# Kernel tuning notes

Measured on AMD Instinct MI355X. Metric: run time of the kernel, lower is better.

Reference implementation:

```python
import jax, jax.numpy as jnp
import numpy as np

B, S, H, NH, L, INTER, WIN = 2, 2048, 512, 8, 4, 2048, 64
HD = H // NH
W1 = WIN // 2          # one-sided window
WB = 2 * W1 + 1        # band width per query
EPS = 1e-12


def layer_norm(x, g, b):
    m = jnp.mean(x, axis=-1, keepdims=True)
    v = jnp.var(x, axis=-1, keepdims=True)
    return (x - m) / jnp.sqrt(v + EPS) * g + b


def setup_inputs() -> dict:
    key = jax.random.key(0)
    ks = jax.random.split(key, 12)
    std = 0.02
    n = lambda k, sh: jax.random.normal(k, sh, jnp.float32) * std
    return {
        "input_embs": jax.random.normal(ks[0], (B, S, H), jnp.float32),
        "attention_mask": jnp.ones((B, S), jnp.float32),
        "pos_emb": n(ks[1], (S, H)),
        "ln_emb_g": jnp.ones((H,), jnp.float32),
        "ln_emb_b": jnp.zeros((H,), jnp.float32),
        "Wq": n(ks[2], (L, H, H)), "bq": jnp.zeros((L, H), jnp.float32),
        "Wk": n(ks[3], (L, H, H)), "bk": jnp.zeros((L, H), jnp.float32),
        "Wv": n(ks[4], (L, H, H)), "bv": jnp.zeros((L, H), jnp.float32),
        "Wo": n(ks[5], (L, H, H)), "bo": jnp.zeros((L, H), jnp.float32),
        "ln1_g": jnp.ones((L, H), jnp.float32), "ln1_b": jnp.zeros((L, H), jnp.float32),
        "Wi": n(ks[6], (L, H, INTER)), "bi": jnp.zeros((L, INTER), jnp.float32),
        "Wo2": n(ks[7], (L, INTER, H)), "bo2": jnp.zeros((L, H), jnp.float32),
        "ln2_g": jnp.ones((L, H), jnp.float32), "ln2_b": jnp.zeros((L, H), jnp.float32),
        "pool_W1": n(ks[8], (H, H)), "pool_b1": jnp.zeros((H,), jnp.float32),
        "pool_W2": n(ks[9], (H, 1)), "pool_b2": jnp.zeros((1,), jnp.float32),
    }


def reference(input_embs, attention_mask, pos_emb, ln_emb_g, ln_emb_b,
              Wq, bq, Wk, bk, Wv, bv, Wo, bo, ln1_g, ln1_b,
              Wi, bi, Wo2, bo2, ln2_g, ln2_b,
              pool_W1, pool_b1, pool_W2, pool_b2):
    # extended additive mask: 0 for attend, -10000 for pad (no global tokens)
    ext = (1.0 - attention_mask) * -10000.0          # [B,S]
    is_masked = ext < 0                              # masked query positions

    # embeddings: input + position, LayerNorm (dropout is identity in eval)
    x = layer_norm(input_embs + pos_emb[None], ln_emb_g, ln_emb_b)

    # sliding-window band indices
    offs = jnp.arange(-W1, W1 + 1)
    idx = jnp.arange(S)[:, None] + offs[None, :]     # [S,WB]
    valid = (idx >= 0) & (idx < S)
    idxc = jnp.clip(idx, 0, S - 1)
    key_bias = ext[:, idxc]                          # [B,S,WB] additive key mask
    scale = 1.0 / jnp.sqrt(jnp.float32(HD))

    def layer(h, p):
        (wq, bq_, wk, bk_, wv, bv_, wo, bo_, g1, b1,
         wi, bi_, wo2, bo2_, g2, b2) = p
        q = (h @ wq + bq_).reshape(B, S, NH, HD) * scale
        k = (h @ wk + bk_).reshape(B, S, NH, HD)
        v = (h @ wv + bv_).reshape(B, S, NH, HD)
        kb = k[:, idxc]                              # [B,S,WB,NH,HD]
        vb = v[:, idxc]
        sc = jnp.einsum('bshd,bswhd->bhsw', q, kb) + key_bias[:, None]
        sc = jnp.where(valid[None, None], sc, -jnp.inf)
        pr = jax.nn.softmax(sc, axis=-1)
        pr = jnp.where(is_masked[:, None, :, None], 0.0, pr)
        ctx = jnp.einsum('bhsw,bswhd->bshd', pr, vb).reshape(B, S, H)
        attn = layer_norm(ctx @ wo + bo_ + h, g1, b1)          # BertSelfOutput
        inter = jax.nn.gelu(attn @ wi + bi_, approximate=False)  # BertIntermediate
        out = layer_norm(inter @ wo2 + bo2_ + attn, g2, b2)      # BertOutput
        return out, None

    params = (Wq, bq, Wk, bk, Wv, bv, Wo, bo, ln1_g, ln1_b,
              Wi, bi, Wo2, bo2, ln2_g, ln2_b)
    x, _ = jax.lax.scan(jax.checkpoint(layer), x, params)

    # AttentionPooling
    e = jnp.tanh(x @ pool_W1 + pool_b1)
    alpha = jnp.exp(e @ pool_W2 + pool_b2) * attention_mask[..., None]  # [B,S,1]
    alpha = alpha / (jnp.sum(alpha, axis=1, keepdims=True) + 1e-8)
    return jnp.einsum('bsh,bs->bh', x, alpha[..., 0])  # [B,H]
```

## Files before the change

### kernel.cpp

```cpp
#include <hip/hip_runtime.h>
#include <hip/hip_bf16.h>
#include <math.h>

#define B_ 2
#define S_ 2048
#define H_ 512
#define NH_ 8
#define HD_ 64
#define L_ 4
#define INTER_ 2048
#define W1_ 32
#define WB_ 65
#define M_ (B_*S_)

typedef __attribute__((ext_vector_type(8))) short short8v;
typedef __attribute__((ext_vector_type(4))) float f32x4;

__device__ __forceinline__ float b2f(ushort u){ return __uint_as_float(((unsigned)u)<<16); }
__device__ __forceinline__ ushort f2b(float f){
  unsigned u = __float_as_uint(f);
  unsigned r = (u + 0x7fffu + ((u>>16)&1u)) >> 16;
  return (ushort)r;
}

__device__ __forceinline__ void async16(const ushort* g, ushort* l){
  __builtin_amdgcn_global_load_lds(
      (const __attribute__((address_space(1))) unsigned int*)g,
      (__attribute__((address_space(3))) unsigned int*)l, 16, 0, 0);
}

__global__ __launch_bounds__(256) void transpose_k(const float* __restrict__ src,
    ushort* __restrict__ dst, int R, int C, size_t sBatch, size_t dBatch)
{
  __shared__ ushort tile[32][33];
  src += (size_t)blockIdx.z * sBatch;
  dst += (size_t)blockIdx.z * dBatch;
  int tx = threadIdx.x & 31, ty = threadIdx.x >> 5;
  int r0 = blockIdx.y * 32, c0 = blockIdx.x * 32;
  #pragma unroll
  for (int i = 0; i < 4; ++i){
    int r = r0 + ty + i*8;
    tile[ty + i*8][tx] = f2b(src[(size_t)r * C + c0 + tx]);
  }
  __syncthreads();
  #pragma unroll
  for (int i = 0; i < 4; ++i){
    int c = c0 + ty + i*8;
    dst[(size_t)c * R + r0 + tx] = tile[tx][ty + i*8];
  }
}

__global__ __launch_bounds__(256) void pack_bqkv(const float* __restrict__ bq,
    const float* __restrict__ bk, const float* __restrict__ bv, float* __restrict__ dst)
{
  int i = blockIdx.x * 256 + threadIdx.x;
  int l = i / 1536, n = i % 1536;
  float v = (n < 512) ? bq[l*512 + n] : (n < 1024 ? bk[l*512 + n - 512] : bv[l*512 + n - 1024]);
  dst[i] = v;
}

template<int EPI>
__global__ __launch_bounds__(256, 4) void gemm_bt(
    const ushort* __restrict__ A, const ushort* __restrict__ Bt,
    const float* __restrict__ bias, ushort* __restrict__ o16,
    float* __restrict__ o32, int M, int N, int K, int Klen)
{
  __shared__ ushort lds_a[2][64][32];
  __shared__ ushort lds_b[2][128][32];
  const int tid = threadIdx.x;
  const int bm = blockIdx.y * 64, bn = blockIdx.x * 128;
  const int kbeg = blockIdx.z * Klen;
  const int wave = tid >> 6, lane = tid & 63;
  const int wr = (wave >> 1) * 32, wc = (wave & 1) * 64;
  const int lr = lane & 15, lg = lane >> 4, lk = lg * 8;
  f32x4 acc[2][4] = {};

  const int srow = tid >> 2, schk = (tid & 3) * 8;
  const ushort* Ag  = A  + (size_t)(bm + srow) * K + kbeg + schk;
  const ushort* Bg0 = Bt + (size_t)(bn + srow) * K + kbeg + schk;
  const ushort* Bg1 = Bt + (size_t)(bn + 64 + srow) * K + kbeg + schk;
  ushort* la = &lds_a[0][0][0] + tid * 8;
  ushort* lb = &lds_b[0][0][0] + tid * 8;

  const int nIter = Klen >> 5;
  async16(Ag, la);
  async16(Bg0, lb);
  async16(Bg1, lb + 2048);
  __syncthreads();

  int cur = 0;
  for (int t = 0; t < nIter; ++t){
    if (t + 1 < nIter){
      int k0 = (t + 1) << 5;
      int nb = cur ^ 1;
      async16(Ag  + k0, la + nb*2048);
      async16(Bg0 + k0, lb + nb*4096);
      async16(Bg1 + k0, lb + nb*4096 + 2048);
    }
    short8v af[2], bfr[4];
    #pragma unroll
    for (int mi = 0; mi < 2; ++mi)
      af[mi] = *(const short8v*)(&lds_a[cur][wr + mi*16 + lr][lk]);
    #pragma unroll
    for (int nj = 0; nj < 4; ++nj)
      bfr[nj] = *(const short8v*)(&lds_b[cur][wc + nj*16 + lr][lk]);
    #pragma unroll
    for (int mi = 0; mi < 2; ++mi)
      #pragma unroll
      for (int nj = 0; nj < 4; ++nj)
        acc[mi][nj] = __builtin_amdgcn_mfma_f32_16x16x32_bf16(af[mi], bfr[nj], acc[mi][nj], 0, 0, 0);
    __syncthreads();
    cur ^= 1;
  }

  const float bscale = (blockIdx.z == 0) ? 1.0f : 0.0f;
  #pragma unroll
  for (int mi = 0; mi < 2; ++mi){
    #pragma unroll
    for (int nj = 0; nj < 4; ++nj){
      int col = bn + wc + nj*16 + lr;
      float bv = bias[col] * bscale;
      #pragma unroll
      for (int j = 0; j < 4; ++j){
        int row = bm + wr + mi*16 + lg*4 + j;
        float v = acc[mi][nj][j] + bv;
        if (EPI == 1) v = 0.5f * v * (1.0f + erff(v * 0.70710678118654752f));
        if (EPI == 2) v = tanhf(v);
        if (EPI == 3) o32[(size_t)blockIdx.z*M*N + (size_t)row * N + col] = v;
        else          o16[(size_t)row * N + col] = f2b(v);
      }
    }
  }
}

__device__ __forceinline__ void block_ln_stats(float v0, float v1, float* red,
                                               float& mean, float& rstd)
{
  int tid = threadIdx.x, wave = tid >> 6, lane = tid & 63;
  float sm = v0 + v1;
  float sq = v0*v0 + v1*v1;
  #pragma unroll
  for (int o = 32; o > 0; o >>= 1){ sm += __shfl_xor(sm, o); sq += __shfl_xor(sq, o); }
  if (lane == 0){ red[wave] = sm; red[4 + wave] = sq; }
  __syncthreads();
  float S = red[0] + red[1] + red[2] + red[3];
  float Q = red[4] + red[5] + red[6] + red[7];
  mean = S * (1.0f / 512.0f);
  float var = Q * (1.0f / 512.0f) - mean*mean;
  if (var < 0.f) var = 0.f;
  rstd = rsqrtf(var + 1e-12f);
}

__global__ __launch_bounds__(256) void embed_ln(const float* __restrict__ x,
    const float* __restrict__ pos, const float* __restrict__ g,
    const float* __restrict__ bb, ushort* __restrict__ out16, float* __restrict__ out32)
{
  __shared__ float red[8];
  int row = blockIdx.x, tid = threadIdx.x;
  int s = row & (S_ - 1);
  float v0 = x[(size_t)row*H_ + tid]       + pos[(size_t)s*H_ + tid];
  float v1 = x[(size_t)row*H_ + tid + 256] + pos[(size_t)s*H_ + tid + 256];
  float mean, rstd;
  block_ln_stats(v0, v1, red, mean, rstd);
  float r0 = (v0 - mean)*rstd*g[tid]       + bb[tid];
  float r1 = (v1 - mean)*rstd*g[tid + 256] + bb[tid + 256];
  out16[(size_t)row*H_ + tid]       = f2b(r0);
  out16[(size_t)row*H_ + tid + 256] = f2b(r1);
  out32[(size_t)row*H_ + tid]       = r0;
  out32[(size_t)row*H_ + tid + 256] = r1;
}

__global__ __launch_bounds__(256) void ln_res(const float* __restrict__ t,
    const float* __restrict__ res, const float* __restrict__ g,
    const float* __restrict__ bb, ushort* __restrict__ out16, float* __restrict__ out32)
{
  __shared__ float red[8];
  int row = blockIdx.x, tid = threadIdx.x;
  const size_t MN = (size_t)M_*H_;
  float v0 = t[(size_t)row*H_ + tid]       + t[MN + (size_t)row*H_ + tid]
           + res[(size_t)row*H_ + tid];
  float v1 = t[(size_t)row*H_ + tid + 256] + t[MN + (size_t)row*H_ + tid + 256]
           + res[(size_t)row*H_ + tid + 256];
  float mean, rstd;
  block_ln_stats(v0, v1, red, mean, rstd);
  float r0 = (v0 - mean)*rstd*g[tid]       + bb[tid];
  float r1 = (v1 - mean)*rstd*g[tid + 256] + bb[tid + 256];
  out16[(size_t)row*H_ + tid]       = f2b(r0);
  out16[(size_t)row*H_ + tid + 256] = f2b(r1);
  out32[(size_t)row*H_ + tid]       = r0;
  out32[(size_t)row*H_ + tid + 256] = r1;
}

__global__ __launch_bounds__(256) void attn_mfma(const ushort* __restrict__ qkv,
    const float* __restrict__ mask, ushort* __restrict__ ctx)
{
  __shared__ ushort K_lds[128][72];
  __shared__ ushort Vt[64][136];
  __shared__ ushort P_lds[64][136];
  __shared__ float  kb[128];

  const int tid = threadIdx.x, wave = tid >> 6, lane = tid & 63;
  const int hh = blockIdx.y & (NH_ - 1), b = blockIdx.y >> 3;
  const int s0 = blockIdx.x * 64;
  const size_t rb = (size_t)b * S_;

  const int ch = tid & 7;
  const int rr = tid >> 3;
  #pragma unroll
  for (int it = 0; it < 4; ++it){
    int c = rr + it*32;
    int j = s0 - 32 + c;
    int jc = min(max(j, 0), S_ - 1);
    const size_t rowb = (rb + jc) * 1536 + hh*64 + ch*8;
    *(short8v*)(&K_lds[c][ch*8]) = *(const short8v*)(qkv + rowb + 512);
    short8v vv = *(const short8v*)(qkv + rowb + 1024);
    #pragma unroll
    for (int t = 0; t < 8; ++t){
      int tt = (t + ch) & 7;
      Vt[ch*8 + tt][c] = (ushort)vv[tt];
    }
  }
  if (tid < 128){
    int j = s0 - 32 + tid;
    kb[tid] = (j >= 0 && j < S_) ? (1.0f - mask[rb + j]) * (-10000.0f) : -1e30f;
  }
  __syncthreads();

  const int wq0 = wave * 16;
  const int lr = lane & 15, lg = lane >> 4, lk = lg * 8;

  const ushort* qbase = qkv + (rb + s0 + wq0 + lr) * 1536 + hh*64;
  short8v aq0 = *(const short8v*)(qbase + lk);
  short8v aq1 = *(const short8v*)(qbase + 32 + lk);

  f32x4 sacc[8];
  #pragma unroll
  for (int cn = 0; cn < 8; ++cn){
    short8v bk0 = *(const short8v*)(&K_lds[cn*16 + lr][lk]);
    short8v bk1 = *(const short8v*)(&K_lds[cn*16 + lr][32 + lk]);
    f32x4 z = {0.f, 0.f, 0.f, 0.f};
    z = __builtin_amdgcn_mfma_f32_16x16x32_bf16(aq0, bk0, z, 0, 0, 0);
    z = __builtin_amdgcn_mfma_f32_16x16x32_bf16(aq1, bk1, z, 0, 0, 0);
    sacc[cn] = z;
  }

  #pragma unroll
  for (int jr = 0; jr < 4; ++jr){
    const int R = wq0 + lg*4 + jr;
    float v[8], mx = -1e30f;
    #pragma unroll
    for (int cn = 0; cn < 8; ++cn){
      int c = cn*16 + lr;
      float sc = sacc[cn][jr] * 0.125f + kb[c];
      if (c < R || c > R + 64) sc = -1e30f;
      v[cn] = sc;
      mx = fmaxf(mx, sc);
    }
    #pragma unroll
    for (int o = 1; o < 16; o <<= 1) mx = fmaxf(mx, __shfl_xor(mx, o));
    float sum = 0.f;
    #pragma unroll
    for (int cn = 0; cn < 8; ++cn){ v[cn] = __expf(v[cn] - mx); sum += v[cn]; }
    #pragma unroll
    for (int o = 1; o < 16; o <<= 1) sum += __shfl_xor(sum, o);
    float qm = mask[rb + s0 + R];
    float inv = ((qm < 0.999f) ? 0.0f : 1.0f) / sum;
    #pragma unroll
    for (int cn = 0; cn < 8; ++cn)
      P_lds[R][cn*16 + lr] = f2b(v[cn] * inv);
  }

  short8v ap[4];
  #pragma unroll
  for (int ks = 0; ks < 4; ++ks)
    ap[ks] = *(const short8v*)(&P_lds[wq0 + lr][ks*32 + lk]);
  #pragma unroll
  for (int dn = 0; dn < 4; ++dn){
    f32x4 z = {0.f, 0.f, 0.f, 0.f};
    #pragma unroll
    for (int ks = 0; ks < 4; ++ks){
      short8v bv = *(const short8v*)(&Vt[dn*16 + lr][ks*32 + lk]);
      z = __builtin_amdgcn_mfma_f32_16x16x32_bf16(ap[ks], bv, z, 0, 0, 0);
    }
    #pragma unroll
    for (int jr = 0; jr < 4; ++jr){
      int R = wq0 + lg*4 + jr;
      ctx[(rb + s0 + R)*H_ + hh*64 + dn*16 + lr] = f2b(z[jr]);
    }
  }
}

__global__ __launch_bounds__(256) void pool_logit(const ushort* __restrict__ e,
    const float* __restrict__ w2, const float* __restrict__ b2p,
    const float* __restrict__ mask, float* __restrict__ alpha)
{
  int tid = threadIdx.x, wave = tid >> 6, lane = tid & 63;
  int r = blockIdx.x * 4 + wave;
  short8v ev = *(const short8v*)(e + (size_t)r*H_ + lane*8);
  float sacc = 0.f;
  #pragma unroll
  for (int j = 0; j < 8; ++j) sacc += b2f((ushort)ev[j]) * w2[lane*8 + j];
  #pragma unroll
  for (int o = 32; o > 0; o >>= 1) sacc += __shfl_xor(sacc, o);
  if (lane == 0){
    float logit = sacc + b2p[0];
    alpha[r] = __expf(logit) * mask[r];
  }
}

__global__ __launch_bounds__(256) void pool_sum(const float* __restrict__ alpha,
                                                float* __restrict__ invsum)
{
  __shared__ float red[4];
  int b = blockIdx.x, tid = threadIdx.x, wave = tid >> 6, lane = tid & 63;
  float s = 0.f;
  for (int k = tid; k < S_; k += 256) s += alpha[b*S_ + k];
  #pragma unroll
  for (int o = 32; o > 0; o >>= 1) s += __shfl_xor(s, o);
  if (lane == 0) red[wave] = s;
  __syncthreads();
  if (tid == 0) invsum[b] = 1.0f / (red[0] + red[1] + red[2] + red[3] + 1e-8f);
}

__global__ __launch_bounds__(256) void pool_wsum(const float* __restrict__ x,
    const float* __restrict__ alpha, float* __restrict__ out_acc)
{
  int chunk = blockIdx.x, b = blockIdx.y, tid = threadIdx.x;
  int s0 = chunk * 128;
  float a0 = 0.f, a1 = 0.f;
  for (int i = 0; i < 128; ++i){
    int srow = s0 + i;
    float al = alpha[b*S_ + srow];
    a0 += x[(size_t)(b*S_ + srow)*H_ + tid]       * al;
    a1 += x[(size_t)(b*S_ + srow)*H_ + tid + 256] * al;
  }
  out_acc[(size_t)chunk*B_*H_ + b*H_ + tid]       = a0;
  out_acc[(size_t)chunk*B_*H_ + b*H_ + tid + 256] = a1;
}

__global__ __launch_bounds__(256) void pool_final(const float* __restrict__ out_acc,
    const float* __restrict__ invsum, float* __restrict__ out)
{
  int i = blockIdx.x * 256 + threadIdx.x;
  if (i < B_*H_){
    int b = i >> 9;
    float s = 0.f;
    #pragma unroll
    for (int c = 0; c < 16; ++c) s += out_acc[(size_t)c*B_*H_ + i];
    out[i] = s * invsum[b];
  }
}

extern "C" void kernel_launch(void* const* d_in, const int* in_sizes, int n_in,
                              void* d_out, int out_size, void* d_ws, size_t ws_size,
                              hipStream_t stream)
{
  const float* input_embs = (const float*)d_in[0];
  const float* mask       = (const float*)d_in[1];
  const float* pos        = (const float*)d_in[2];
  const float* ln_emb_g   = (const float*)d_in[3];
  const float* ln_emb_b   = (const float*)d_in[4];
  const float* Wq  = (const float*)d_in[5];
  const float* bq  = (const float*)d_in[6];
  const float* Wk  = (const float*)d_in[7];
  const float* bk  = (const float*)d_in[8];
  const float* Wv  = (const float*)d_in[9];
  const float* bv  = (const float*)d_in[10];
  const float* Wo  = (const float*)d_in[11];
  const float* bo  = (const float*)d_in[12];
  const float* ln1_g = (const float*)d_in[13];
  const float* ln1_b = (const float*)d_in[14];
  const float* Wi  = (const float*)d_in[15];
  const float* bi  = (const float*)d_in[16];
  const float* Wo2 = (const float*)d_in[17];
  const float* bo2 = (const float*)d_in[18];
  const float* ln2_g = (const float*)d_in[19];
  const float* ln2_b = (const float*)d_in[20];
  const float* pW1 = (const float*)d_in[21];
  const float* pb1 = (const float*)d_in[22];
  const float* pW2 = (const float*)d_in[23];
  const float* pb2 = (const float*)d_in[24];

  char* ws = (char*)d_ws;
  size_t off = 0;
  auto alloc = [&](size_t bytes)->char*{
    char* p = ws + off; off += (bytes + 255) & ~(size_t)255; return p;
  };
  ushort* WqkvT  = (ushort*)alloc((size_t)L_*1536*512*2);
  ushort* WoT    = (ushort*)alloc((size_t)L_*512*512*2);
  ushort* WiT    = (ushort*)alloc((size_t)L_*2048*512*2);
  ushort* Wo2T   = (ushort*)alloc((size_t)L_*512*2048*2);
  ushort* pW1T   = (ushort*)alloc((size_t)512*512*2);
  float*  bqkv   = (float*)alloc((size_t)L_*1536*4);
  ushort* h16    = (ushort*)alloc((size_t)M_*H_*2);
  float*  h32    = (float*)alloc((size_t)M_*H_*4);
  ushort* qkv    = (ushort*)alloc((size_t)M_*1536*2);
  ushort* ctx    = (ushort*)alloc((size_t)M_*H_*2);
  ushort* attn16 = (ushort*)alloc((size_t)M_*H_*2);
  float*  attn32 = (float*)alloc((size_t)M_*H_*4);
  ushort* inter  = (ushort*)alloc((size_t)M_*INTER_*2);
  float*  t1     = (float*)alloc((size_t)2*M_*H_*4);
  float*  alpha  = (float*)alloc((size_t)M_*4);
  float*  invsum = (float*)alloc(256);
  float*  outacc = (float*)alloc((size_t)16*B_*H_*4);

  dim3 tb(256);
  transpose_k<<<dim3(16,16,L_), tb, 0, stream>>>(Wq, WqkvT,            512,  512, (size_t)512*512,  (size_t)1536*512);
  transpose_k<<<dim3(16,16,L_), tb, 0, stream>>>(Wk, WqkvT + 512*512,  512,  512, (size_t)512*512,  (size_t)1536*512);
  transpose_k<<<dim3(16,16,L_), tb, 0, stream>>>(Wv, WqkvT + 1024*512, 512,  512, (size_t)512*512,  (size_t)1536*512);
  transpose_k<<<dim3(16,16,L_), tb, 0, stream>>>(Wo, WoT,              512,  512, (size_t)512*512,  (size_t)512*512);
  transpose_k<<<dim3(64,16,L_), tb, 0, stream>>>(Wi, WiT,              512, 2048, (size_t)512*2048, (size_t)2048*512);
  transpose_k<<<dim3(16,64,L_), tb, 0, stream>>>(Wo2, Wo2T,           2048,  512, (size_t)2048*512, (size_t)512*2048);
  transpose_k<<<dim3(16,16,1),  tb, 0, stream>>>(pW1, pW1T,            512,  512, 0, 0);
  pack_bqkv<<<dim3(L_*1536/256), tb, 0, stream>>>(bq, bk, bv, bqkv);

  embed_ln<<<dim3(M_), tb, 0, stream>>>(input_embs, pos, ln_emb_g, ln_emb_b, h16, h32);

  for (int l = 0; l < L_; ++l){
    gemm_bt<0><<<dim3(12,64,1), tb, 0, stream>>>(h16, WqkvT + (size_t)l*1536*512, bqkv + l*1536,
                                                 qkv, nullptr, M_, 1536, 512, 512);
    attn_mfma<<<dim3(S_/64, B_*NH_), tb, 0, stream>>>(qkv, mask, ctx);
    gemm_bt<3><<<dim3(4,64,2), tb, 0, stream>>>(ctx, WoT + (size_t)l*512*512, bo + l*512,
                                                nullptr, t1, M_, 512, 512, 256);
    ln_res<<<dim3(M_), tb, 0, stream>>>(t1, h32, ln1_g + l*512, ln1_b + l*512, attn16, attn32);
    gemm_bt<1><<<dim3(16,64,1), tb, 0, stream>>>(attn16, WiT + (size_t)l*2048*512, bi + l*2048,
                                                 inter, nullptr, M_, 2048, 512, 512);
    gemm_bt<3><<<dim3(4,64,2), tb, 0, stream>>>(inter, Wo2T + (size_t)l*512*2048, bo2 + l*512,
                                                nullptr, t1, M_, 512, 2048, 1024);
    ln_res<<<dim3(M_), tb, 0, stream>>>(t1, attn32, ln2_g + l*512, ln2_b + l*512, h16, h32);
  }

  gemm_bt<2><<<dim3(4,64,1), tb, 0, stream>>>(h16, pW1T, pb1, ctx, nullptr, M_, 512, 512, 512);
  pool_logit<<<dim3(M_/4), tb, 0, stream>>>(ctx, pW2, pb2, mask, alpha);
  pool_sum<<<dim3(B_), tb, 0, stream>>>(alpha, invsum);
  pool_wsum<<<dim3(16, B_), tb, 0, stream>>>(h32, alpha, outacc);
  pool_final<<<dim3((B_*H_ + 255)/256), tb, 0, stream>>>(outacc, invsum, (float*)d_out);
}
```

Baseline: 440.8 us.

## Enlarge GEMM tiles to 128x128 and fuse Wo projection with residual LayerNorm

The generic bf16 MFMA GEMM moves from 64x128 to 128x128 block tiles, with each wave computing a 64x64 sub-tile, and grids are halved in M. This gives more reuse per LDS load but fewer blocks and more registers, and the occupancy hint is dropped. The attention output projection is replaced by a new kernel that computes full 16-row x 512-column output tiles. It applies bias, residual and LayerNorm in the epilogue, removing the split-K fp32 round trip through t1 and one separate ln_res launch per layer.

Result: slower. 475.2 us (+7.8%).

```diff
diff --git a/kernel.cpp b/kernel.cpp
--- a/kernel.cpp
+++ b/kernel.cpp
@@ -60,32 +60,31 @@
 }
 
 template<int EPI>
-__global__ __launch_bounds__(256, 4) void gemm_bt(
+__global__ __launch_bounds__(256) void gemm_bt(
     const ushort* __restrict__ A, const ushort* __restrict__ Bt,
     const float* __restrict__ bias, ushort* __restrict__ o16,
     float* __restrict__ o32, int M, int N, int K, int Klen)
 {
-  __shared__ ushort lds_a[2][64][32];
+  __shared__ ushort lds_a[2][128][32];
   __shared__ ushort lds_b[2][128][32];
   const int tid = threadIdx.x;
-  const int bm = blockIdx.y * 64, bn = blockIdx.x * 128;
+  const int bm = blockIdx.y * 128, bn = blockIdx.x * 128;
   const int kbeg = blockIdx.z * Klen;
   const int wave = tid >> 6, lane = tid & 63;
-  const int wr = (wave >> 1) * 32, wc = (wave & 1) * 64;
+  const int wr = (wave >> 1) * 64, wc = (wave & 1) * 64;
   const int lr = lane & 15, lg = lane >> 4, lk = lg * 8;
-  f32x4 acc[2][4] = {};
-
-  const int srow = tid >> 2, schk = (tid & 3) * 8;
-  const ushort* Ag  = A  + (size_t)(bm + srow) * K + kbeg + schk;
-  const ushort* Bg0 = Bt + (size_t)(bn + srow) * K + kbeg + schk;
-  const ushort* Bg1 = Bt + (size_t)(bn + 64 + srow) * K + kbeg + schk;
+  f32x4 acc[4][4] = {};
+
+  const ushort* Ag = A  + (size_t)(bm + (tid >> 2)) * K + kbeg + (tid & 3) * 8;
+  const ushort* Bg = Bt + (size_t)(bn + (tid >> 2)) * K + kbeg + (tid & 3) * 8;
   ushort* la = &lds_a[0][0][0] + tid * 8;
   ushort* lb = &lds_b[0][0][0] + tid * 8;
 
   const int nIter = Klen >> 5;
-  async16(Ag, la);
-  async16(Bg0, lb);
-  async16(Bg1, lb + 2048);
+  async16(Ag,            la);
+  async16(Ag + 64 * K,   la + 2048);
+  async16(Bg,            lb);
+  async16(Bg + 64 * K,   lb + 2048);
   __syncthreads();
 
   int cur = 0;
@@ -93,19 +92,20 @@
     if (t + 1 < nIter){
       int k0 = (t + 1) << 5;
       int nb = cur ^ 1;
-      async16(Ag  + k0, la + nb*2048);
-      async16(Bg0 + k0, lb + nb*4096);
-      async16(Bg1 + k0, lb + nb*4096 + 2048);
-    }
-    short8v af[2], bfr[4];
-    #pragma unroll
-    for (int mi = 0; mi < 2; ++mi)
+      async16(Ag + k0,          la + nb*4096);
+      async16(Ag + 64*K + k0,   la + nb*4096 + 2048);
+      async16(Bg + k0,          lb + nb*4096);
+      async16(Bg + 64*K + k0,   lb + nb*4096 + 2048);
+    }
+    short8v af[4], bfr[4];
+    #pragma unroll
+    for (int mi = 0; mi < 4; ++mi)
       af[mi] = *(const short8v*)(&lds_a[cur][wr + mi*16 + lr][lk]);
     #pragma unroll
     for (int nj = 0; nj < 4; ++nj)
       bfr[nj] = *(const short8v*)(&lds_b[cur][wc + nj*16 + lr][lk]);
     #pragma unroll
-    for (int mi = 0; mi < 2; ++mi)
+    for (int mi = 0; mi < 4; ++mi)
       #pragma unroll
       for (int nj = 0; nj < 4; ++nj)
         acc[mi][nj] = __builtin_amdgcn_mfma_f32_16x16x32_bf16(af[mi], bfr[nj], acc[mi][nj], 0, 0, 0);
@@ -115,7 +115,7 @@
 
   const float bscale = (blockIdx.z == 0) ? 1.0f : 0.0f;
   #pragma unroll
-  for (int mi = 0; mi < 2; ++mi){
+  for (int mi = 0; mi < 4; ++mi){
     #pragma unroll
     for (int nj = 0; nj < 4; ++nj){
       int col = bn + wc + nj*16 + lr;
@@ -129,6 +129,109 @@
         if (EPI == 3) o32[(size_t)blockIdx.z*M*N + (size_t)row * N + col] = v;
         else          o16[(size_t)row * N + col] = f2b(v);
       }
+    }
+  }
+}
+
+__global__ __launch_bounds__(256) void gemm_wo_ln(
+    const ushort* __restrict__ A, const ushort* __restrict__ Bt,
+    const float* __restrict__ bias, const float* __restrict__ res,
+    const float* __restrict__ g, const float* __restrict__ bb,
+    ushort* __restrict__ out16, float* __restrict__ out32)
+{
+  __shared__ ushort lds_a[2][16][32];
+  __shared__ ushort lds_b[2][512][32];
+  __shared__ float  red[4][2][16];
+
+  const int tid = threadIdx.x;
+  const int bm = blockIdx.x * 16;
+  const int wave = tid >> 6, lane = tid & 63;
+  const int wc = wave * 128;
+  const int lr = lane & 15, lg = lane >> 4, lk = lg * 8;
+  f32x4 acc[8] = {};
+
+  const ushort* Ag = A  + (size_t)(bm + (tid >> 2)) * 512 + (tid & 3) * 8;
+  const ushort* Bg = Bt + (size_t)(tid >> 2) * 512 + (tid & 3) * 8;
+  ushort* la = &lds_a[0][0][0] + tid * 8;
+  ushort* lb = &lds_b[0][0][0] + tid * 8;
+
+  if (tid < 64) async16(Ag, la);
+  #pragma unroll
+  for (int r = 0; r < 8; ++r) async16(Bg + (size_t)r*64*512, lb + r*2048);
+  __syncthreads();
+
+  int cur = 0;
+  for (int t = 0; t < 16; ++t){
+    if (t < 15){
+      int k0 = (t + 1) * 32;
+      int nb = cur ^ 1;
+      if (tid < 64) async16(Ag + k0, la + nb*512);
+      #pragma unroll
+      for (int r = 0; r < 8; ++r)
+        async16(Bg + (size_t)r*64*512 + k0, lb + nb*16384 + r*2048);
+    }
+    short8v af = *(const short8v*)(&lds_a[cur][lr][lk]);
+    #pragma unroll
+    for (int nj = 0; nj < 8; ++nj){
+      short8v bf = *(const short8v*)(&lds_b[cur][wc + nj*16 + lr][lk]);
+      acc[nj] = __builtin_amdgcn_mfma_f32_16x16x32_bf16(af, bf, acc[nj], 0, 0, 0);
+    }
+    __syncthreads();
+    cur ^= 1;
+  }
+
+  float vv[8][4];
+  float sm[4] = {0,0,0,0}, sq[4] = {0,0,0,0};
+  #pragma unroll
+  for (int nj = 0; nj < 8; ++nj){
+    int col = wc + nj*16 + lr;
+    float bv = bias[col];
+    #pragma unroll
+    for (int j = 0; j < 4; ++j){
+      int grow = bm + lg*4 + j;
+      float v = acc[nj][j] + bv + res[(size_t)grow*512 + col];
+      vv[nj][j] = v;
+      sm[j] += v;
+      sq[j] += v*v;
+    }
+  }
+  #pragma unroll
+  for (int o = 1; o < 16; o <<= 1){
+    #pragma unroll
+    for (int j = 0; j < 4; ++j){
+      sm[j] += __shfl_xor(sm[j], o);
+      sq[j] += __shfl_xor(sq[j], o);
+    }
+  }
+  if (lr == 0){
+    #pragma unroll
+    for (int j = 0; j < 4; ++j){
+      red[wave][0][lg*4 + j] = sm[j];
+      red[wave][1][lg*4 + j] = sq[j];
+    }
+  }
+  __syncthreads();
+  float mean[4], rstd[4];
+  #pragma unroll
+  for (int j = 0; j < 4; ++j){
+    int R = lg*4 + j;
+    float S = red[0][0][R] + red[1][0][R] + red[2][0][R] + red[3][0][R];
+    float Q = red[0][1][R] + red[1][1][R] + red[2][1][R] + red[3][1][R];
+    mean[j] = S * (1.0f / 512.0f);
+    float var = Q * (1.0f / 512.0f) - mean[j]*mean[j];
+    if (var < 0.f) var = 0.f;
+    rstd[j] = rsqrtf(var + 1e-12f);
+  }
+  #pragma unroll
+  for (int nj = 0; nj < 8; ++nj){
+    int col = wc + nj*16 + lr;
+    float gv = g[col], bbv = bb[col];
+    #pragma unroll
+    for (int j = 0; j < 4; ++j){
+      int grow = bm + lg*4 + j;
+      float o = (vv[nj][j] - mean[j]) * rstd[j] * gv + bbv;
+      out16[(size_t)grow*512 + col] = f2b(o);
+      out32[(size_t)grow*512 + col] = o;
     }
   }
 }
@@ -417,20 +520,19 @@
   embed_ln<<<dim3(M_), tb, 0, stream>>>(input_embs, pos, ln_emb_g, ln_emb_b, h16, h32);
 
   for (int l = 0; l < L_; ++l){
-    gemm_bt<0><<<dim3(12,64,1), tb, 0, stream>>>(h16, WqkvT + (size_t)l*1536*512, bqkv + l*1536,
+    gemm_bt<0><<<dim3(12,32,1), tb, 0, stream>>>(h16, WqkvT + (size_t)l*1536*512, bqkv + l*1536,
                                                  qkv, nullptr, M_, 1536, 512, 512);
     attn_mfma<<<dim3(S_/64, B_*NH_), tb, 0, stream>>>(qkv, mask, ctx);
-    gemm_bt<3><<<dim3(4,64,2), tb, 0, stream>>>(ctx, WoT + (size_t)l*512*512, bo + l*512,
-                                                nullptr, t1, M_, 512, 512, 256);
-    ln_res<<<dim3(M_), tb, 0, stream>>>(t1, h32, ln1_g + l*512, ln1_b + l*512, attn16, attn32);
-    gemm_bt<1><<<dim3(16,64,1), tb, 0, stream>>>(attn16, WiT + (size_t)l*2048*512, bi + l*2048,
+    gemm_wo_ln<<<dim3(M_/16), tb, 0, stream>>>(ctx, WoT + (size_t)l*512*512, bo + l*512,
+                                               h32, ln1_g + l*512, ln1_b + l*512, attn16, attn32);
+    gemm_bt<1><<<dim3(16,32,1), tb, 0, stream>>>(attn16, WiT + (size_t)l*2048*512, bi + l*2048,
                                                  inter, nullptr, M_, 2048, 512, 512);
-    gemm_bt<3><<<dim3(4,64,2), tb, 0, stream>>>(inter, Wo2T + (size_t)l*512*2048, bo2 + l*512,
+    gemm_bt<3><<<dim3(4,32,2), tb, 0, stream>>>(inter, Wo2T + (size_t)l*512*2048, bo2 + l*512,
                                                 nullptr, t1, M_, 512, 2048, 1024);
     ln_res<<<dim3(M_), tb, 0, stream>>>(t1, attn32, ln2_g + l*512, ln2_b + l*512, h16, h32);
   }
 
-  gemm_bt<2><<<dim3(4,64,1), tb, 0, stream>>>(h16, pW1T, pb1, ctx, nullptr, M_, 512, 512, 512);
+  gemm_bt<2><<<dim3(4,32,1), tb, 0, stream>>>(h16, pW1T, pb1, ctx, nullptr, M_, 512, 512, 512);
   pool_logit<<<dim3(M_/4), tb, 0, stream>>>(ctx, pW2, pb2, mask, alpha);
   pool_sum<<<dim3(B_), tb, 0, stream>>>(alpha, invsum);
   pool_wsum<<<dim3(16, B_), tb, 0, stream>>>(h32, alpha, outacc);
```

## Triple-buffer GEMM LDS with swizzle and vectorize LayerNorm/pool loads

Applied to the files above, without the earlier changes.

The GEMM mainloop changes from double to triple buffering. It issues tiles two steps ahead and uses explicit vmcnt waits and raw s_barriers in place of __syncthreads. An XOR swizzle on the LDS k-chunk index is applied on both the async write side and the fragment read side to reduce LDS bank conflicts. Separately, the LayerNorm and pooling kernels switch to float2 vectorized loads and stores over adjacent column pairs. Together this raises LDS use and ties correctness to hand-counted vmcnt values.

Result: faster. 415.8 us (-5.7%).

```diff
diff --git a/kernel.cpp b/kernel.cpp
--- a/kernel.cpp
+++ b/kernel.cpp
@@ -65,52 +65,58 @@
     const float* __restrict__ bias, ushort* __restrict__ o16,
     float* __restrict__ o32, int M, int N, int K, int Klen)
 {
-  __shared__ ushort lds_a[2][64][32];
-  __shared__ ushort lds_b[2][128][32];
+  __shared__ ushort lds[3*6144];
   const int tid = threadIdx.x;
   const int bm = blockIdx.y * 64, bn = blockIdx.x * 128;
   const int kbeg = blockIdx.z * Klen;
   const int wave = tid >> 6, lane = tid & 63;
   const int wr = (wave >> 1) * 32, wc = (wave & 1) * 64;
-  const int lr = lane & 15, lg = lane >> 4, lk = lg * 8;
+  const int lr = lane & 15, lg = lane >> 4;
+  const int lkS = (lg ^ ((lr >> 1) & 3)) * 8;
   f32x4 acc[2][4] = {};
 
-  const int srow = tid >> 2, schk = (tid & 3) * 8;
+  const int srow = tid >> 2;
+  const int schk = (((tid & 3) ^ ((tid >> 3) & 3))) * 8;
   const ushort* Ag  = A  + (size_t)(bm + srow) * K + kbeg + schk;
   const ushort* Bg0 = Bt + (size_t)(bn + srow) * K + kbeg + schk;
   const ushort* Bg1 = Bt + (size_t)(bn + 64 + srow) * K + kbeg + schk;
-  ushort* la = &lds_a[0][0][0] + tid * 8;
-  ushort* lb = &lds_b[0][0][0] + tid * 8;
 
   const int nIter = Klen >> 5;
-  async16(Ag, la);
-  async16(Bg0, lb);
-  async16(Bg1, lb + 2048);
-  __syncthreads();
-
-  int cur = 0;
+  auto issueTile = [&](int t, int buf){
+    int k0 = t << 5;
+    ushort* d = &lds[0] + buf*6144 + tid*8;
+    async16(Ag  + k0, d);
+    async16(Bg0 + k0, d + 2048);
+    async16(Bg1 + k0, d + 4096);
+  };
+
+  issueTile(0, 0);
+  issueTile(1, 1);
+
+  int cb = 0;
   for (int t = 0; t < nIter; ++t){
-    if (t + 1 < nIter){
-      int k0 = (t + 1) << 5;
-      int nb = cur ^ 1;
-      async16(Ag  + k0, la + nb*2048);
-      async16(Bg0 + k0, lb + nb*4096);
-      async16(Bg1 + k0, lb + nb*4096 + 2048);
-    }
+    int ib = cb + 2; if (ib >= 3) ib -= 3;
+    if (t + 2 < nIter) issueTile(t + 2, ib);
+    if (t + 2 < nIter)      asm volatile("s_waitcnt vmcnt(6)" ::: "memory");
+    else if (t + 1 < nIter) asm volatile("s_waitcnt vmcnt(3)" ::: "memory");
+    else                    asm volatile("s_waitcnt vmcnt(0)" ::: "memory");
+    __builtin_amdgcn_sched_barrier(0);
+    __builtin_amdgcn_s_barrier();
+    const ushort* bufp = &lds[0] + cb*6144;
     short8v af[2], bfr[4];
     #pragma unroll
     for (int mi = 0; mi < 2; ++mi)
-      af[mi] = *(const short8v*)(&lds_a[cur][wr + mi*16 + lr][lk]);
+      af[mi] = *(const short8v*)(bufp + (wr + mi*16 + lr)*32 + lkS);
     #pragma unroll
     for (int nj = 0; nj < 4; ++nj)
-      bfr[nj] = *(const short8v*)(&lds_b[cur][wc + nj*16 + lr][lk]);
+      bfr[nj] = *(const short8v*)(bufp + 2048 + (wc + nj*16 + lr)*32 + lkS);
     #pragma unroll
     for (int mi = 0; mi < 2; ++mi)
       #pragma unroll
       for (int nj = 0; nj < 4; ++nj)
         acc[mi][nj] = __builtin_amdgcn_mfma_f32_16x16x32_bf16(af[mi], bfr[nj], acc[mi][nj], 0, 0, 0);
-    __syncthreads();
-    cur ^= 1;
+    __builtin_amdgcn_s_barrier();
+    cb = cb + 1; if (cb == 3) cb = 0;
   }
 
   const float bscale = (blockIdx.z == 0) ? 1.0f : 0.0f;
@@ -158,16 +164,20 @@
   __shared__ float red[8];
   int row = blockIdx.x, tid = threadIdx.x;
   int s = row & (S_ - 1);
-  float v0 = x[(size_t)row*H_ + tid]       + pos[(size_t)s*H_ + tid];
-  float v1 = x[(size_t)row*H_ + tid + 256] + pos[(size_t)s*H_ + tid + 256];
+  const size_t base = (size_t)row*H_ + tid*2;
+  float2 xv = *(const float2*)(x + base);
+  float2 pv = *(const float2*)(pos + (size_t)s*H_ + tid*2);
+  float v0 = xv.x + pv.x, v1 = xv.y + pv.y;
   float mean, rstd;
   block_ln_stats(v0, v1, red, mean, rstd);
-  float r0 = (v0 - mean)*rstd*g[tid]       + bb[tid];
-  float r1 = (v1 - mean)*rstd*g[tid + 256] + bb[tid + 256];
-  out16[(size_t)row*H_ + tid]       = f2b(r0);
-  out16[(size_t)row*H_ + tid + 256] = f2b(r1);
-  out32[(size_t)row*H_ + tid]       = r0;
-  out32[(size_t)row*H_ + tid + 256] = r1;
+  float2 gv = *(const float2*)(g + tid*2);
+  float2 bv = *(const float2*)(bb + tid*2);
+  float r0 = (v0 - mean)*rstd*gv.x + bv.x;
+  float r1 = (v1 - mean)*rstd*gv.y + bv.y;
+  ushort2 o2; o2.x = f2b(r0); o2.y = f2b(r1);
+  *(ushort2*)(out16 + base) = o2;
+  float2 f2v; f2v.x = r0; f2v.y = r1;
+  *(float2*)(out32 + base) = f2v;
 }
 
 __global__ __launch_bounds__(256) void ln_res(const float* __restrict__ t,
@@ -177,18 +187,22 @@
   __shared__ float red[8];
   int row = blockIdx.x, tid = threadIdx.x;
   const size_t MN = (size_t)M_*H_;
-  float v0 = t[(size_t)row*H_ + tid]       + t[MN + (size_t)row*H_ + tid]
-           + res[(size_t)row*H_ + tid];
-  float v1 = t[(size_t)row*H_ + tid + 256] + t[MN + (size_t)row*H_ + tid + 256]
-           + res[(size_t)row*H_ + tid + 256];
+  const size_t base = (size_t)row*H_ + tid*2;
+  float2 t0 = *(const float2*)(t + base);
+  float2 t1v = *(const float2*)(t + MN + base);
+  float2 rv = *(const float2*)(res + base);
+  float v0 = t0.x + t1v.x + rv.x;
+  float v1 = t0.y + t1v.y + rv.y;
   float mean, rstd;
   block_ln_stats(v0, v1, red, mean, rstd);
-  float r0 = (v0 - mean)*rstd*g[tid]       + bb[tid];
-  float r1 = (v1 - mean)*rstd*g[tid + 256] + bb[tid + 256];
-  out16[(size_t)row*H_ + tid]       = f2b(r0);
-  out16[(size_t)row*H_ + tid + 256] = f2b(r1);
-  out32[(size_t)row*H_ + tid]       = r0;
-  out32[(size_t)row*H_ + tid + 256] = r1;
+  float2 gv = *(const float2*)(g + tid*2);
+  float2 bv = *(const float2*)(bb + tid*2);
+  float r0 = (v0 - mean)*rstd*gv.x + bv.x;
+  float r1 = (v1 - mean)*rstd*gv.y + bv.y;
+  ushort2 o2; o2.x = f2b(r0); o2.y = f2b(r1);
+  *(ushort2*)(out16 + base) = o2;
+  float2 f2v; f2v.x = r0; f2v.y = r1;
+  *(float2*)(out32 + base) = f2v;
 }
 
 __global__ __launch_bounds__(256) void attn_mfma(const ushort* __restrict__ qkv,
@@ -327,15 +341,17 @@
 {
   int chunk = blockIdx.x, b = blockIdx.y, tid = threadIdx.x;
   int s0 = chunk * 128;
+  int c0 = tid * 2;
   float a0 = 0.f, a1 = 0.f;
   for (int i = 0; i < 128; ++i){
     int srow = s0 + i;
     float al = alpha[b*S_ + srow];
-    a0 += x[(size_t)(b*S_ + srow)*H_ + tid]       * al;
-    a1 += x[(size_t)(b*S_ + srow)*H_ + tid + 256] * al;
-  }
-  out_acc[(size_t)chunk*B_*H_ + b*H_ + tid]       = a0;
-  out_acc[(size_t)chunk*B_*H_ + b*H_ + tid + 256] = a1;
+    float2 xv = *(const float2*)(x + (size_t)(b*S_ + srow)*H_ + c0);
+    a0 += xv.x * al;
+    a1 += xv.y * al;
+  }
+  float2 o; o.x = a0; o.y = a1;
+  *(float2*)(out_acc + (size_t)chunk*B_*H_ + b*H_ + c0) = o;
 }
 
 __global__ __launch_bounds__(256) void pool_final(const float* __restrict__ out_acc,
```
